# Kernel optimization log

Measured on AMD Instinct MI355X. Metric: run time of the kernel, lower is better.

Reference implementation:

```python
import jax, jax.numpy as jnp
import numpy as np

N = 10000      # nodes
E = 160000     # edges
F = 64         # channels (hidden_irreps 0e multiplicity)
NS = 10        # species
NB = 8         # num_bessel
NL = 4         # max_ell + 1
LM = 16        # total SH components (l=0..3)
RMAX = 10.0
AVG = 16.0     # avg_num_neighbors
L_OF = jnp.array([0,1,1,1,2,2,2,2,2,3,3,3,3,3,3,3])  # l index of each SH component


def _sph(u):
    """Component-normalized real spherical harmonics l=0..3 on unit vectors [E,3] -> [E,16]."""
    x, y, z = u[..., 0], u[..., 1], u[..., 2]
    s3, s5, s7 = 3.0**0.5, 5.0**0.5, 7.0**0.5
    s15, s42, s70, s105 = 15.0**0.5, 42.0**0.5, 70.0**0.5, 105.0**0.5
    one = jnp.ones_like(x)
    return jnp.stack([
        one,
        s3*x, s3*y, s3*z,
        s15*x*y, s15*y*z, (s5/2)*(3*z*z - 1), s15*x*z, (s15/2)*(x*x - y*y),
        (s70/4)*y*(3*x*x - y*y), s105*x*y*z, (s42/4)*y*(5*z*z - 1),
        (s7/2)*z*(5*z*z - 3), (s42/4)*x*(5*z*z - 1),
        (s105/2)*z*(x*x - y*y), (s70/4)*x*(x*x - 3*y*y),
    ], axis=-1)


def _bessel(r):
    """Bessel radial basis with smooth polynomial cutoff. r [E] -> [E,NB]."""
    n = jnp.arange(1, NB + 1, dtype=r.dtype)
    eb = (2.0 / RMAX) ** 0.5 * jnp.sin(n * jnp.pi * r[:, None] / RMAX) / (r[:, None] + 1e-9)
    p = 5.0
    xr = r / RMAX
    env = (1.0 - ((p+1)*(p+2)/2) * xr**p + p*(p+2) * xr**(p+1) - (p*(p+1)/2) * xr**(p+2))
    env = jnp.where(xr < 1.0, env, 0.0)
    return eb * env[:, None]


def _interaction(node_feats, node_attrs, Y, bess, senders, receivers,
                 W_up, Wr1, Wr2, Wr3, W_mix, W_sc, w_prod, last):
    # linear down-projection of scalar channel feeding the edge tensor product
    h = node_feats[:, :, 0] @ W_up                                   # [N,F]
    # per-edge radial weights, one per (channel, l) path
    R = jax.nn.silu(bess @ Wr1)
    R = jax.nn.silu(R @ Wr2)
    R = (R @ Wr3).reshape(E, F, NL)                                  # [E,F,4]
    Rlm = R[:, :, L_OF]                                              # [E,F,16]
    # edge tensor-product message: gather senders, modulate by radial, outer with SH
    m = h[senders][:, :, None] * Rlm * Y[:, None, :]                 # [E,F,16]
    A = jax.ops.segment_sum(m, receivers, num_segments=N) / AVG      # [N,F,16]
    # per-l channel mixing (equivariant linear)
    A = jnp.einsum('nfk,kfg->ngk', A, W_mix[L_OF])                   # [N,F,16]
    # species-dependent residual (skip tensor product with node attrs)
    wsp = jnp.einsum('ns,sfg->nfg', node_attrs, W_sc)                # [N,F,F]
    sc = jnp.einsum('nfk,nfg->ngk', node_feats, wsp)                 # [N,F,16]
    # symmetric product basis (correlation=3): scalar-modulated polynomial, equivariant
    s = A[:, :, 0]
    B = A * (w_prod[0] + w_prod[1]*s + w_prod[2]*s*s)[:, :, None]
    out = B + sc
    if last:  # last layer keeps only 0e (scalar) irreps
        out = out * (jnp.arange(LM) == 0).astype(out.dtype)
    return out


def _forward(positions, node_attrs, shifts, senders, receivers, w_embed,
             u0_up, u0_r1, u0_r2, u0_r3, u0_mix, u0_sc, u0_prod, w_read0,
             u1_up, u1_r1, u1_r2, u1_r3, u1_mix, u1_sc, u1_prod, w_mlp1, w_mlp2):
    vec = positions[receivers] - positions[senders] + shifts         # [E,3]
    r = jnp.linalg.norm(vec, axis=-1)
    Y = _sph(vec / (r[:, None] + 1e-9))                              # [E,16]
    bess = _bessel(r)                                                # [E,8]
    # node embedding into scalar channel of [N,F,16] state
    nf = jnp.zeros((N, F, LM), positions.dtype).at[:, :, 0].set(node_attrs @ w_embed)
    nf = _interaction(nf, node_attrs, Y, bess, senders, receivers,
                      u0_up, u0_r1, u0_r2, u0_r3, u0_mix, u0_sc, u0_prod, last=False)
    out0 = nf[:, :, 0] @ w_read0                                     # [N,1] linear readout
    nf = _interaction(nf, node_attrs, Y, bess, senders, receivers,
                      u1_up, u1_r1, u1_r2, u1_r3, u1_mix, u1_sc, u1_prod, last=True)
    out1 = jax.nn.silu(nf[:, :, 0] @ w_mlp1) @ w_mlp2                # [N,1] nonlinear readout
    return jnp.stack([out0, out1], axis=1)                           # [N,2,1]


def setup_inputs() -> dict:
    key = jax.random.key(0)
    ks = jax.random.split(key, 24)
    positions = jax.random.uniform(ks[0], (N, 3), jnp.float32) * 5.0
    species = jax.random.randint(ks[1], (N,), 0, NS)
    node_attrs = jax.nn.one_hot(species, NS, dtype=jnp.float32)
    shifts = jnp.zeros((E, 3), jnp.float32)
    senders = jax.random.randint(ks[2], (E,), 0, N, dtype=jnp.int32)
    receivers = jax.random.randint(ks[3], (E,), 0, N, dtype=jnp.int32)

    def nrm(k, shape, fan_in):
        return jax.random.normal(k, shape, jnp.float32) / (fan_in ** 0.5)

    d = dict(positions=positions, node_attrs=node_attrs, shifts=shifts,
             senders=senders, receivers=receivers,
             w_embed=nrm(ks[4], (NS, F), NS))
    for i, base in ((0, 5), (1, 13)):
        d[f'u{i}_up'] = nrm(ks[base], (F, F), F)
        d[f'u{i}_r1'] = nrm(ks[base+1], (NB, 64), NB)
        d[f'u{i}_r2'] = nrm(ks[base+2], (64, 64), 64)
        d[f'u{i}_r3'] = nrm(ks[base+3], (64, F*NL), 64)
        d[f'u{i}_mix'] = nrm(ks[base+4], (NL, F, F), F)
        d[f'u{i}_sc'] = nrm(ks[base+5], (NS, F, F), F)
        d[f'u{i}_prod'] = nrm(ks[base+6], (3, F), 1)
    d['w_read0'] = nrm(ks[12], (F, 1), F)
    d['w_mlp1'] = nrm(ks[20], (F, 16), F)
    d['w_mlp2'] = nrm(ks[21], (16, 1), 16)
    return d


def reference(positions, node_attrs, shifts, senders, receivers, w_embed,
              u0_up, u0_r1, u0_r2, u0_r3, u0_mix, u0_sc, u0_prod, w_read0,
              u1_up, u1_r1, u1_r2, u1_r3, u1_mix, u1_sc, u1_prod, w_mlp1, w_mlp2):
    return _forward(positions, node_attrs, shifts, senders, receivers, w_embed,
                    u0_up, u0_r1, u0_r2, u0_r3, u0_mix, u0_sc, u0_prod, w_read0,
                    u1_up, u1_r1, u1_r2, u1_r3, u1_mix, u1_sc, u1_prod, w_mlp1, w_mlp2)
```

## Files before the change

### kernel.cpp

```cpp
#include <hip/hip_runtime.h>
#include <hip/hip_bf16.h>
#include <cstdint>
#include <cstddef>

#define NN 10000
#define NE 160000

typedef unsigned short u16;
typedef __attribute__((ext_vector_type(8))) short short8;
typedef __attribute__((ext_vector_type(4))) float f32x4;

__device__ __forceinline__ float b2f(u16 u){
    union { uint32_t i; float f; } v; v.i = ((uint32_t)u) << 16; return v.f;
}
__device__ __forceinline__ u16 f2b(float f){
    union { __hip_bfloat16 h; u16 u; } c; c.h = __float2bfloat16(f); return c.u;
}
__device__ __forceinline__ float silu_f(float x){ return x / (1.f + __expf(-x)); }
__device__ __forceinline__ float ldr(const void* p, int i, int bf){
    return bf ? b2f(((const u16*)p)[i]) : ((const float*)p)[i];
}

constexpr size_t W_FLAG = 0;
constexpr size_t W_CNT  = 16;
constexpr size_t W_OFFS = 10016;
constexpr size_t W_CUR  = 20032;
constexpr size_t W_SSND = 30032;
constexpr size_t W_ATT  = 350032;
constexpr size_t W_POS  = 450032;
constexpr size_t W_SHF  = 480032;
constexpr size_t W_WGT  = 960032;
constexpr size_t OW_EMB = 0;
constexpr size_t OW_UP0 = 640;
constexpr size_t OW_R10 = 4736;
constexpr size_t OW_R20 = 5248;
constexpr size_t OW_R30 = 9344;
constexpr size_t OW_MIX0= 25728;
constexpr size_t OW_SC0 = 42112;
constexpr size_t OW_PR0 = 83072;
constexpr size_t OW_UP1 = 83264;
constexpr size_t OW_R11 = 87360;
constexpr size_t OW_R21 = 87872;
constexpr size_t OW_R31 = 91968;
constexpr size_t OW_MIX1= 108352;
constexpr size_t OW_SC1 = 124736;
constexpr size_t OW_PR1 = 165696;
constexpr size_t OW_RD0 = 165888;
constexpr size_t OW_ML1 = 165952;
constexpr size_t OW_ML2 = 166976;
constexpr size_t OW_TEND = 167000;
constexpr size_t W_BES  = W_WGT + OW_TEND;
constexpr size_t W_NF0  = W_BES + (size_t)NE*8;
constexpr size_t W_H    = W_NF0 + (size_t)NN*64;
constexpr size_t W_A    = W_H   + (size_t)NN*64;
constexpr size_t W_NF1  = W_A   + (size_t)NN*64;
constexpr size_t W_R0   = W_NF1 + (size_t)NN*64;
constexpr size_t W_R1   = W_R0  + (size_t)NE*32;
constexpr size_t WP_DUAL   = W_R1 + (size_t)NE*32;
constexpr size_t WP_SINGLE = W_R0 + (size_t)NE*32;
constexpr size_t W_RS_D = WP_DUAL   + 10400;
constexpr size_t W_RS_S = WP_SINGLE + 10400;
constexpr size_t W_RS_F = W_R0;
constexpr size_t WP_F   = W_R0 + NE;

constexpr size_t NEED_DUAL   = (W_RS_D + NE) * 4;
constexpr size_t NEED_SINGLE = (W_RS_S + NE) * 4;

constexpr int OCT  = 520;
constexpr int OCTS = 136;

__global__ void k_dh(const uint32_t* __restrict__ attrs, const int* __restrict__ rcv,
                     int* __restrict__ flag, int* __restrict__ cnt){
    int i = blockIdx.x * 256 + threadIdx.x;
    int c = 0;
    if (i < 50000){
        uint32_t v = attrs[i];
        c = (v != 0u && v != 0x3F800000u) ? 1 : 0;
    }
    unsigned long long m = __ballot(c);
    if ((threadIdx.x & 63) == 0 && m)
        atomicAdd(flag, (int)__popcll(m));
    if (i < NE) atomicAdd(&cnt[rcv[i]], 1);
}

struct PrepArgs { const void* s[21]; float* d[21]; int n[21]; };
__global__ __launch_bounds__(1024) void k_scan_prep(PrepArgs a, const int* __restrict__ flag,
        const int* __restrict__ cnt, int* __restrict__ offs, int* __restrict__ cur,
        u16* __restrict__ WP, float* __restrict__ nf0, float* __restrict__ h){
    int bf = flag[0] > 100;
    int t = threadIdx.x;
    if (blockIdx.x == 0){
        __shared__ int cl[10000];
        __shared__ int part[1024];
        for (int i = t; i < 10000; i += 1024) cl[i] = cnt[i];
        __syncthreads();
        int base = t * 10;
        int s = 0;
        #pragma unroll
        for (int i = 0; i < 10; i++) if (base + i < NN) s += cl[base + i];
        part[t] = s; __syncthreads();
        for (int d = 1; d < 1024; d <<= 1){
            int v = part[t];
            if (t >= d) v += part[t - d];
            __syncthreads();
            part[t] = v;
            __syncthreads();
        }
        int run = part[t] - s;
        #pragma unroll
        for (int i = 0; i < 10; i++){
            int idx = base + i;
            if (idx < NN){ offs[idx] = run; cur[idx] = run; run += cl[idx]; }
        }
        if (t == 1023) offs[NN] = part[1023];
    } else if (blockIdx.x < 65){
        int stride = 64 * 1024;
        int t0 = (blockIdx.x - 1) * 1024 + t;
        for (int k = 0; k < 21; k++){
            float* d = a.d[k]; int n4 = a.n[k] >> 2;
            if (bf){
                const uint2* s = (const uint2*)a.s[k];
                for (int i = t0; i < n4; i += stride){
                    uint2 v = s[i];
                    float4 o;
                    o.x = b2f((u16)(v.x & 0xffffu));
                    o.y = b2f((u16)(v.x >> 16));
                    o.z = b2f((u16)(v.y & 0xffffu));
                    o.w = b2f((u16)(v.y >> 16));
                    ((float4*)d)[i] = o;
                }
            } else {
                const float4* s = (const float4*)a.s[k];
                for (int i = t0; i < n4; i += stride) ((float4*)d)[i] = s[i];
            }
        }
    } else if (blockIdx.x < 67){
        int b = blockIdx.x - 65;
        const void* W1 = a.s[b ? 12 : 5];
        const void* W2 = a.s[b ? 13 : 6];
        const void* W3 = a.s[b ? 14 : 7];
        u16* dst = WP + b * 10400;
        for (int i = t; i < 5200; i += 1024) ((uint32_t*)dst)[i] = 0;
        __syncthreads();
        for (int i = t; i < 512; i += 1024){
            int n = i >> 3, k = i & 7;
            dst[n*8 + k] = f2b(ldr(W1, k*64 + n, bf));
        }
        for (int i = t; i < 2048; i += 1024){
            int k = (i >> 6) * 2, n = i & 63;
            uint32_t p2 = ((uint32_t)f2b(ldr(W2, (k+1)*64 + n, bf)) << 16) | f2b(ldr(W2, k*64 + n, bf));
            uint32_t p3 = ((uint32_t)f2b(ldr(W3, (k+1)*256 + 4*n, bf)) << 16) | f2b(ldr(W3, k*256 + 4*n, bf));
            *(uint32_t*)&dst[2080 + (k>>3)*OCT + n*8 + (k&7)] = p2;
            *(uint32_t*)&dst[6240 + (k>>3)*OCT + n*8 + (k&7)] = p3;
        }
    } else {
        int nb = blockIdx.x - 67;
        int n = nb*16 + (t >> 6);
        int l = t & 63;
        const void* attrs = a.s[1];
        const void* Wemb  = a.s[3];
        const void* Wup0  = a.s[4];
        float acc = 0.f;
        #pragma unroll
        for (int s = 0; s < 10; s++) acc += ldr(attrs, n*10 + s, bf) * ldr(Wemb, s*64 + l, bf);
        nf0[n*64 + l] = acc;
        float hv = 0.f;
        #pragma unroll 16
        for (int g = 0; g < 64; g++) hv += __shfl(acc, g) * ldr(Wup0, g*64 + l, bf);
        h[n*64 + l] = hv;
    }
}

__global__ void k_scatter_r(const int* __restrict__ rcv, const int* __restrict__ snd,
        const void* __restrict__ posr, const void* __restrict__ shfr,
        int* __restrict__ cur, int* __restrict__ ssnd, float* __restrict__ rs,
        const int* __restrict__ flag){
    int e = blockIdx.x * 256 + threadIdx.x;
    if (e >= NE) return;
    int bf = flag[0] > 100;
    int r = rcv[e], s = snd[e];
    float vx = ldr(posr, r*3+0, bf) - ldr(posr, s*3+0, bf) + ldr(shfr, e*3+0, bf);
    float vy = ldr(posr, r*3+1, bf) - ldr(posr, s*3+1, bf) + ldr(shfr, e*3+1, bf);
    float vz = ldr(posr, r*3+2, bf) - ldr(posr, s*3+2, bf) + ldr(shfr, e*3+2, bf);
    float rr = sqrtf(vx*vx + vy*vy + vz*vz);
    int p = atomicAdd(&cur[r], 1);
    ssnd[p] = s;
    rs[p] = rr;
}

__global__ void k_bess(const float* __restrict__ rs, float* __restrict__ bessp){
    int p = blockIdx.x * 256 + threadIdx.x;
    if (p >= NE) return;
    float rr = rs[p];
    float xr = rr * 0.1f;
    float x2 = xr*xr; float x5 = x2*x2*xr;
    float env = 1.f - 21.f*x5 + 35.f*x5*xr - 15.f*x5*x2;
    if (xr >= 1.f) env = 0.f;
    float scl = 0.4472135954999579f * env / (rr + 1e-9f);
    float b[8];
    #pragma unroll
    for (int n = 1; n <= 8; n++)
        b[n-1] = scl * sinf((float)n * 3.14159265358979323846f * rr * 0.1f);
    float4* be = (float4*)(bessp + (size_t)p*8);
    be[0] = make_float4(b[0], b[1], b[2], b[3]);
    be[1] = make_float4(b[4], b[5], b[6], b[7]);
}

__global__ __launch_bounds__(256) void k_mlp_mfma(const float* __restrict__ rs,
        const u16* __restrict__ WPa, const u16* __restrict__ WPb,
        u16* __restrict__ R0, u16* __restrict__ R1, int nblk0){
    __shared__ __align__(16) u16 W[10400];
    __shared__ __align__(16) u16 X[4][20*OCTS];
    int half = blockIdx.x >= nblk0;
    int blk  = half ? blockIdx.x - nblk0 : blockIdx.x;
    const u16* WP = half ? WPb : WPa;
    u16* R = half ? R1 : R0;
    int t = threadIdx.x;
    int w = t >> 6, lane = t & 63;
    int q = lane >> 4, r = lane & 15;
    u16* Xw = &X[w][0];
    for (int i = t; i < 1300; i += 256) ((uint4*)W)[i] = ((const uint4*)WP)[i];
    {
        uint32_t* xz = (uint32_t*)(Xw + OCTS);
        for (int i = lane; i < 204; i += 64) xz[i] = 0;
    }
    __syncthreads();
    int pbase = blk * 256 + w * 64;
    #pragma unroll 1
    for (int st = 0; st < 4; st++){
        int pb = pbase + st * 16;
        {
            float rr = rs[pb + (lane >> 2)];
            float xr = rr * 0.1f;
            float x2 = xr*xr, x5 = x2*x2*xr;
            float env = 1.f - 21.f*x5 + 35.f*x5*xr - 15.f*x5*x2;
            if (xr >= 1.f) env = 0.f;
            float scl = 0.4472135954999579f * env / (rr + 1e-9f);
            int k0 = (lane & 3) * 2;
            float b0 = scl * __sinf((float)(k0+1) * 0.3141592653589793f * rr);
            float b1 = scl * __sinf((float)(k0+2) * 0.3141592653589793f * rr);
            ((uint32_t*)Xw)[lane] = ((uint32_t)f2b(b1) << 16) | f2b(b0);
        }
        {
            short8 a = *(const short8*)&Xw[q*OCTS + r*8];
            #pragma unroll
            for (int nt = 0; nt < 4; nt++){
                short8 b = *(const short8*)&W[q*OCT + (nt*16 + r)*8];
                f32x4 c = {0.f, 0.f, 0.f, 0.f};
                c = __builtin_amdgcn_mfma_f32_16x16x32_bf16(a, b, c, 0, 0, 0);
                #pragma unroll
                for (int g = 0; g < 4; g++){
                    int e = q*4 + g;
                    int n = nt*16 + r;
                    Xw[(4 + (n>>3))*OCTS + e*8 + (n&7)] = f2b(silu_f(c[g]));
                }
            }
        }
        {
            short8 a0 = *(const short8*)&Xw[(4+q)*OCTS + r*8];
            short8 a1 = *(const short8*)&Xw[(8+q)*OCTS + r*8];
            #pragma unroll
            for (int nt = 0; nt < 4; nt++){
                short8 b0 = *(const short8*)&W[2080 + q*OCT + (nt*16 + r)*8];
                short8 b1 = *(const short8*)&W[2080 + (4+q)*OCT + (nt*16 + r)*8];
                f32x4 c = {0.f, 0.f, 0.f, 0.f};
                c = __builtin_amdgcn_mfma_f32_16x16x32_bf16(a0, b0, c, 0, 0, 0);
                c = __builtin_amdgcn_mfma_f32_16x16x32_bf16(a1, b1, c, 0, 0, 0);
                #pragma unroll
                for (int g = 0; g < 4; g++){
                    int e = q*4 + g;
                    int n = nt*16 + r;
                    Xw[(12 + (n>>3))*OCTS + e*8 + (n&7)] = f2b(silu_f(c[g]));
                }
            }
        }
        {
            short8 a0 = *(const short8*)&Xw[(12+q)*OCTS + r*8];
            short8 a1 = *(const short8*)&Xw[(16+q)*OCTS + r*8];
            #pragma unroll
            for (int nt = 0; nt < 4; nt++){
                short8 b0 = *(const short8*)&W[6240 + q*OCT + (nt*16 + r)*8];
                short8 b1 = *(const short8*)&W[6240 + (4+q)*OCT + (nt*16 + r)*8];
                f32x4 c = {0.f, 0.f, 0.f, 0.f};
                c = __builtin_amdgcn_mfma_f32_16x16x32_bf16(a0, b0, c, 0, 0, 0);
                c = __builtin_amdgcn_mfma_f32_16x16x32_bf16(a1, b1, c, 0, 0, 0);
                #pragma unroll
                for (int g = 0; g < 4; g++){
                    int e = q*4 + g;
                    int n = nt*16 + r;
                    R[(size_t)(pb + e)*64 + n] = f2b(c[g]);
                }
            }
        }
    }
}

template<int LAST>
__global__ __launch_bounds__(256) void k_gnode(const int* __restrict__ offs,
        const int* __restrict__ ssnd, const float* __restrict__ h, const u16* __restrict__ R,
        const float* __restrict__ nf, const float* __restrict__ attrs,
        const float* __restrict__ Wmix0, const float* __restrict__ Wsc,
        const float* __restrict__ Wprod, const float* __restrict__ Wtail,
        const float* __restrict__ Wml2, const float* __restrict__ Wup1,
        float* __restrict__ nf1out, float* __restrict__ hout,
        void* __restrict__ out, const int* __restrict__ flag){
    int wv = threadIdx.x >> 6;
    int n  = blockIdx.x * 4 + wv;
    int l  = threadIdx.x & 63;
    int beg = __builtin_amdgcn_readfirstlane(offs[n]);
    int end = __builtin_amdgcn_readfirstlane(offs[n+1]);
    float acc = 0.f;
    for (int c = beg; c < end; c += 64){
        int ld = c + l; if (ld >= end) ld = end - 1;
        int sv = ssnd[ld];
        int m = end - c; if (m > 64) m = 64;
        int j = 0;
        for (; j + 4 <= m; j += 4){
            int s0 = __builtin_amdgcn_readlane(sv, j+0);
            int s1 = __builtin_amdgcn_readlane(sv, j+1);
            int s2 = __builtin_amdgcn_readlane(sv, j+2);
            int s3 = __builtin_amdgcn_readlane(sv, j+3);
            float r0 = b2f(R[(size_t)(c+j+0)*64 + l]);
            float r1 = b2f(R[(size_t)(c+j+1)*64 + l]);
            float r2 = b2f(R[(size_t)(c+j+2)*64 + l]);
            float r3 = b2f(R[(size_t)(c+j+3)*64 + l]);
            acc += h[s0*64 + l]*r0 + h[s1*64 + l]*r1 + h[s2*64 + l]*r2 + h[s3*64 + l]*r3;
        }
        for (; j < m; j++){
            int s = __builtin_amdgcn_readlane(sv, j);
            acc += h[s*64 + l] * b2f(R[(size_t)(c+j)*64 + l]);
        }
    }
    float Af  = acc * 0.0625f;
    float nff = nf[n*64 + l];
    float am = 0.f;
    #pragma unroll 16
    for (int f = 0; f < 64; f++) am += __shfl(Af, f) * Wmix0[f*64 + l];
    float sc = 0.f;
    for (int s = 0; s < 10; s++){
        float av = attrs[n*10 + s];
        if (av != 0.f){
            const float* Ws = Wsc + s*4096;
            float t = 0.f;
            #pragma unroll 16
            for (int f = 0; f < 64; f++) t += __shfl(nff, f) * Ws[f*64 + l];
            sc += av * t;
        }
    }
    float poly = Wprod[l] + Wprod[64 + l]*am + Wprod[128 + l]*am*am;
    float val = am*poly + sc;
    float rv;
    if (LAST == 0){
        nf1out[n*64 + l] = val;
        float hv = 0.f;
        #pragma unroll 16
        for (int g = 0; g < 64; g++) hv += __shfl(val, g) * Wup1[g*64 + l];
        hout[n*64 + l] = hv;
        rv = val * Wtail[l];
    } else {
        int lj = l & 15;
        float t = 0.f;
        #pragma unroll 16
        for (int g = 0; g < 64; g++){
            float vg = __shfl(val, g);
            t += vg * Wtail[g*16 + lj];
        }
        rv = (l < 16) ? (silu_f(t) * Wml2[lj]) : 0.f;
    }
    #pragma unroll
    for (int o2 = 32; o2; o2 >>= 1) rv += __shfl_down(rv, o2);
    if (l == 0){
        int idx = 2*n + LAST;
        if (flag[0] > 100) ((__hip_bfloat16*)out)[idx] = __float2bfloat16(rv);
        else               ((float*)out)[idx] = rv;
    }
}

__global__ __launch_bounds__(256) void k_msg_fused(const int* __restrict__ offs,
        const int* __restrict__ ssnd, const float* __restrict__ h, const float* __restrict__ bessp,
        const float* __restrict__ W1, const float* __restrict__ W2, const float* __restrict__ W3,
        float* __restrict__ A){
    int wv = threadIdx.x >> 6;
    int n  = blockIdx.x * 4 + wv;
    int l  = threadIdx.x & 63;
    float w1c[8];
    #pragma unroll
    for (int i = 0; i < 8; i++) w1c[i] = W1[i*64 + l];
    float w2c[64];
    #pragma unroll
    for (int j = 0; j < 64; j++) w2c[j] = W2[j*64 + l];
    float w3c[64];
    #pragma unroll
    for (int j = 0; j < 64; j++) w3c[j] = W3[j*256 + 4*l];
    float acc = 0.f;
    int beg = __builtin_amdgcn_readfirstlane(offs[n]);
    int end = __builtin_amdgcn_readfirstlane(offs[n+1]);
    for (int p = beg; p < end; p++){
        int s = __builtin_amdgcn_readfirstlane(ssnd[p]);
        const float* be = bessp + (size_t)p*8;
        float h1 = 0.f;
        #pragma unroll
        for (int i = 0; i < 8; i++) h1 += be[i] * w1c[i];
        h1 = silu_f(h1);
        float h2 = 0.f;
        #pragma unroll
        for (int j = 0; j < 64; j++) h2 += __shfl(h1, j) * w2c[j];
        h2 = silu_f(h2);
        float rr = 0.f;
        #pragma unroll
        for (int j = 0; j < 64; j++) rr += __shfl(h2, j) * w3c[j];
        acc += h[s*64 + l] * rr;
    }
    A[n*64 + l] = acc * 0.0625f;
}
template<int LAST>
__global__ __launch_bounds__(256) void k_node(const float* __restrict__ A, const float* __restrict__ nf,
        const float* __restrict__ attrs, const float* __restrict__ Wmix0, const float* __restrict__ Wsc,
        const float* __restrict__ Wprod, const float* __restrict__ Wtail, const float* __restrict__ Wml2,
        const float* __restrict__ Wup1, float* __restrict__ nf1out, float* __restrict__ hout,
        void* __restrict__ out, const int* __restrict__ flag){
    int wv = threadIdx.x >> 6;
    int n  = blockIdx.x * 4 + wv;
    int l  = threadIdx.x & 63;
    float Af  = A[n*64 + l];
    float nff = nf[n*64 + l];
    float am = 0.f;
    #pragma unroll 16
    for (int f = 0; f < 64; f++) am += __shfl(Af, f) * Wmix0[f*64 + l];
    float sc = 0.f;
    for (int s = 0; s < 10; s++){
        float av = attrs[n*10 + s];
        if (av != 0.f){
            const float* Ws = Wsc + s*4096;
            float t = 0.f;
            #pragma unroll 16
            for (int f = 0; f < 64; f++) t += __shfl(nff, f) * Ws[f*64 + l];
            sc += av * t;
        }
    }
    float poly = Wprod[l] + Wprod[64 + l]*am + Wprod[128 + l]*am*am;
    float val = am*poly + sc;
    float rv;
    if (LAST == 0){
        nf1out[n*64 + l] = val;
        float hv = 0.f;
        #pragma unroll 16
        for (int g = 0; g < 64; g++) hv += __shfl(val, g) * Wup1[g*64 + l];
        hout[n*64 + l] = hv;
        rv = val * Wtail[l];
    } else {
        int lj = l & 15;
        float t = 0.f;
        #pragma unroll 16
        for (int g = 0; g < 64; g++){
            float vg = __shfl(val, g);
            t += vg * Wtail[g*16 + lj];
        }
        rv = (l < 16) ? (silu_f(t) * Wml2[lj]) : 0.f;
    }
    #pragma unroll
    for (int o2 = 32; o2; o2 >>= 1) rv += __shfl_down(rv, o2);
    if (l == 0){
        int idx = 2*n + LAST;
        if (flag[0] > 100) ((__hip_bfloat16*)out)[idx] = __float2bfloat16(rv);
        else               ((float*)out)[idx] = rv;
    }
}

extern "C" void kernel_launch(void* const* d_in, const int* in_sizes, int n_in,
                              void* d_out, int out_size, void* d_ws, size_t ws_size,
                              hipStream_t stream) {
    int*   iw = (int*)d_ws;
    float* fw = (float*)d_ws;
    const int* snd = (const int*)d_in[3];
    const int* rcv = (const int*)d_in[4];

    PrepArgs pa;
    const int    pidx[21] = {0,1,2, 5,6,7,8,9,10,11,12,13,14,15,16,17,18,19,20,21,22};
    const size_t pdst[21] = {W_POS, W_ATT, W_SHF,
        W_WGT+OW_EMB, W_WGT+OW_UP0, W_WGT+OW_R10, W_WGT+OW_R20, W_WGT+OW_R30,
        W_WGT+OW_MIX0, W_WGT+OW_SC0, W_WGT+OW_PR0,
        W_WGT+OW_UP1, W_WGT+OW_R11, W_WGT+OW_R21, W_WGT+OW_R31,
        W_WGT+OW_MIX1, W_WGT+OW_SC1, W_WGT+OW_PR1,
        W_WGT+OW_RD0, W_WGT+OW_ML1, W_WGT+OW_ML2};
    const int    pn[21]   = {30000, 100000, 480000,
        640, 4096, 512, 4096, 16384, 16384, 40960, 192,
        4096, 512, 4096, 16384, 16384, 40960, 192, 64, 1024, 16};
    for (int i = 0; i < 21; i++){
        pa.s[i] = d_in[pidx[i]];
        pa.d[i] = fw + pdst[i];
        pa.n[i] = pn[i];
    }

    const int dual   = (ws_size >= NEED_DUAL);
    const int single = (!dual && ws_size >= NEED_SINGLE);
    const size_t wp  = dual ? WP_DUAL : (single ? WP_SINGLE : WP_F);
    const size_t wrs = dual ? W_RS_D  : (single ? W_RS_S  : W_RS_F);

    hipMemsetAsync(iw, 0, (W_CNT + NN) * sizeof(int), stream);
    k_dh<<<NE/256, 256, 0, stream>>>((const uint32_t*)d_in[1], rcv, iw + W_FLAG, iw + W_CNT);
    k_scan_prep<<<692, 1024, 0, stream>>>(pa, iw + W_FLAG, iw + W_CNT, iw + W_OFFS, iw + W_CUR,
                                          (u16*)(fw + wp), fw + W_NF0, fw + W_H);
    k_scatter_r<<<NE/256, 256, 0, stream>>>(rcv, snd, d_in[0], d_in[2],
                                            iw + W_CUR, iw + W_SSND, fw + wrs, iw + W_FLAG);

    if (dual){
        k_mlp_mfma<<<1250, 256, 0, stream>>>(fw + wrs, (const u16*)(fw + wp),
                                             (const u16*)(fw + wp) + 10400,
                                             (u16*)(fw + W_R0), (u16*)(fw + W_R1), 625);
        k_gnode<0><<<NN/4, 256, 0, stream>>>(iw+W_OFFS, iw+W_SSND, fw+W_H, (const u16*)(fw+W_R0),
            fw+W_NF0, fw+W_ATT, fw+W_WGT+OW_MIX0, fw+W_WGT+OW_SC0, fw+W_WGT+OW_PR0,
            fw+W_WGT+OW_RD0, nullptr, fw+W_WGT+OW_UP1, fw+W_NF1, fw+W_A, d_out, iw+W_FLAG);
        k_gnode<1><<<NN/4, 256, 0, stream>>>(iw+W_OFFS, iw+W_SSND, fw+W_A, (const u16*)(fw+W_R1),
            fw+W_NF1, fw+W_ATT, fw+W_WGT+OW_MIX1, fw+W_WGT+OW_SC1, fw+W_WGT+OW_PR1,
            fw+W_WGT+OW_ML1, fw+W_WGT+OW_ML2, nullptr, nullptr, nullptr, d_out, iw+W_FLAG);
    } else if (single){
        k_mlp_mfma<<<625, 256, 0, stream>>>(fw + wrs, (const u16*)(fw + wp),
                                            (const u16*)(fw + wp),
                                            (u16*)(fw + W_R0), (u16*)(fw + W_R0), 2000000);
        k_gnode<0><<<NN/4, 256, 0, stream>>>(iw+W_OFFS, iw+W_SSND, fw+W_H, (const u16*)(fw+W_R0),
            fw+W_NF0, fw+W_ATT, fw+W_WGT+OW_MIX0, fw+W_WGT+OW_SC0, fw+W_WGT+OW_PR0,
            fw+W_WGT+OW_RD0, nullptr, fw+W_WGT+OW_UP1, fw+W_NF1, fw+W_A, d_out, iw+W_FLAG);
        k_mlp_mfma<<<625, 256, 0, stream>>>(fw + wrs, (const u16*)(fw + wp) + 10400,
                                            (const u16*)(fw + wp) + 10400,
                                            (u16*)(fw + W_R0), (u16*)(fw + W_R0), 2000000);
        k_gnode<1><<<NN/4, 256, 0, stream>>>(iw+W_OFFS, iw+W_SSND, fw+W_A, (const u16*)(fw+W_R0),
            fw+W_NF1, fw+W_ATT, fw+W_WGT+OW_MIX1, fw+W_WGT+OW_SC1, fw+W_WGT+OW_PR1,
            fw+W_WGT+OW_ML1, fw+W_WGT+OW_ML2, nullptr, nullptr, nullptr, d_out, iw+W_FLAG);
    } else {
        k_bess<<<NE/256, 256, 0, stream>>>(fw + wrs, fw + W_BES);
        k_msg_fused<<<NN/4, 256, 0, stream>>>(iw+W_OFFS, iw+W_SSND, fw+W_H, fw+W_BES,
                                              fw+W_WGT+OW_R10, fw+W_WGT+OW_R20,
                                              fw+W_WGT+OW_R30, fw + W_A);
        k_node<0><<<NN/4, 256, 0, stream>>>(fw + W_A, fw + W_NF0, fw + W_ATT,
                                            fw + W_WGT + OW_MIX0, fw + W_WGT + OW_SC0,
                                            fw + W_WGT + OW_PR0, fw + W_WGT + OW_RD0, nullptr,
                                            fw + W_WGT + OW_UP1, fw + W_NF1, fw + W_H,
                                            d_out, iw + W_FLAG);
        k_msg_fused<<<NN/4, 256, 0, stream>>>(iw+W_OFFS, iw+W_SSND, fw+W_H, fw+W_BES,
                                              fw+W_WGT+OW_R11, fw+W_WGT+OW_R21,
                                              fw+W_WGT+OW_R31, fw + W_A);
        k_node<1><<<NN/4, 256, 0, stream>>>(fw + W_A, fw + W_NF1, fw + W_ATT,
                                            fw + W_WGT + OW_MIX1, fw + W_WGT + OW_SC1,
                                            fw + W_WGT + OW_PR1, fw + W_WGT + OW_ML1,
                                            fw + W_WGT + OW_ML2, nullptr, nullptr, nullptr,
                                            d_out, iw + W_FLAG);
    }
}
```

Measured before the change: 224.2 us.

## Fuse front-end memset, histogram, scan, prep and scatter into one cooperative kernel

```diff
diff --git a/kernel.cpp b/kernel.cpp
--- a/kernel.cpp
+++ b/kernel.cpp
@@ -1,10 +1,15 @@
 #include <hip/hip_runtime.h>
 #include <hip/hip_bf16.h>
+#include <hip/hip_cooperative_groups.h>
 #include <cstdint>
 #include <cstddef>
 
+namespace cg = cooperative_groups;
+
 #define NN 10000
 #define NE 160000
+#define FGRID 1024
+#define FGT   (FGRID * 256)
 
 typedef unsigned short u16;
 typedef __attribute__((ext_vector_type(8))) short short8;
@@ -69,37 +74,43 @@
 constexpr int OCT  = 520;
 constexpr int OCTS = 136;
 
-__global__ void k_dh(const uint32_t* __restrict__ attrs, const int* __restrict__ rcv,
-                     int* __restrict__ flag, int* __restrict__ cnt){
-    int i = blockIdx.x * 256 + threadIdx.x;
-    int c = 0;
-    if (i < 50000){
-        uint32_t v = attrs[i];
-        c = (v != 0u && v != 0x3F800000u) ? 1 : 0;
-    }
-    unsigned long long m = __ballot(c);
-    if ((threadIdx.x & 63) == 0 && m)
-        atomicAdd(flag, (int)__popcll(m));
-    if (i < NE) atomicAdd(&cnt[rcv[i]], 1);
-}
-
 struct PrepArgs { const void* s[21]; float* d[21]; int n[21]; };
-__global__ __launch_bounds__(1024) void k_scan_prep(PrepArgs a, const int* __restrict__ flag,
-        const int* __restrict__ cnt, int* __restrict__ offs, int* __restrict__ cur,
-        u16* __restrict__ WP, float* __restrict__ nf0, float* __restrict__ h){
+
+__global__ __launch_bounds__(256, 4) void k_front(PrepArgs a,
+        const int* __restrict__ rcv, const int* __restrict__ snd,
+        int* __restrict__ iw0, int* __restrict__ offs, int* __restrict__ rank,
+        int* __restrict__ ssnd, float* __restrict__ rs,
+        u16* __restrict__ WP, float* __restrict__ nf0, float* __restrict__ h)
+{
+    cg::grid_group grid = cg::this_grid();
+    int t = threadIdx.x;
+    int gtid = blockIdx.x * 256 + t;
+    int* flag = iw0;
+    int* cnt  = iw0 + 16;
+
+    for (int i = gtid; i < 10016; i += FGT) iw0[i] = 0;
+    grid.sync();
+
+    {
+        int c = 0;
+        if (gtid < 50000){
+            uint32_t v = ((const uint32_t*)a.s[1])[gtid];
+            c = (v != 0u && v != 0x3F800000u) ? 1 : 0;
+        }
+        unsigned long long m = __ballot(c);
+        if ((t & 63) == 0 && m) atomicAdd(flag, (int)__popcll(m));
+        if (gtid < NE) rank[gtid] = atomicAdd(&cnt[rcv[gtid]], 1);
+    }
+    grid.sync();
     int bf = flag[0] > 100;
-    int t = threadIdx.x;
+
     if (blockIdx.x == 0){
-        __shared__ int cl[10000];
-        __shared__ int part[1024];
-        for (int i = t; i < 10000; i += 1024) cl[i] = cnt[i];
-        __syncthreads();
-        int base = t * 10;
+        __shared__ int part[256];
+        int base = t * 40;
         int s = 0;
-        #pragma unroll
-        for (int i = 0; i < 10; i++) if (base + i < NN) s += cl[base + i];
+        for (int i = 0; i < 40; i++){ int idx = base + i; if (idx < NN) s += cnt[idx]; }
         part[t] = s; __syncthreads();
-        for (int d = 1; d < 1024; d <<= 1){
+        for (int d = 1; d < 256; d <<= 1){
             int v = part[t];
             if (t >= d) v += part[t - d];
             __syncthreads();
@@ -107,46 +118,24 @@
             __syncthreads();
         }
         int run = part[t] - s;
-        #pragma unroll
-        for (int i = 0; i < 10; i++){
+        for (int i = 0; i < 40; i++){
             int idx = base + i;
-            if (idx < NN){ offs[idx] = run; cur[idx] = run; run += cl[idx]; }
-        }
-        if (t == 1023) offs[NN] = part[1023];
-    } else if (blockIdx.x < 65){
-        int stride = 64 * 1024;
-        int t0 = (blockIdx.x - 1) * 1024 + t;
-        for (int k = 0; k < 21; k++){
-            float* d = a.d[k]; int n4 = a.n[k] >> 2;
-            if (bf){
-                const uint2* s = (const uint2*)a.s[k];
-                for (int i = t0; i < n4; i += stride){
-                    uint2 v = s[i];
-                    float4 o;
-                    o.x = b2f((u16)(v.x & 0xffffu));
-                    o.y = b2f((u16)(v.x >> 16));
-                    o.z = b2f((u16)(v.y & 0xffffu));
-                    o.w = b2f((u16)(v.y >> 16));
-                    ((float4*)d)[i] = o;
-                }
-            } else {
-                const float4* s = (const float4*)a.s[k];
-                for (int i = t0; i < n4; i += stride) ((float4*)d)[i] = s[i];
-            }
-        }
-    } else if (blockIdx.x < 67){
-        int b = blockIdx.x - 65;
+            if (idx < NN){ offs[idx] = run; run += cnt[idx]; }
+        }
+        if (t == 255) offs[NN] = part[255];
+    } else if (blockIdx.x <= 2){
+        int b = blockIdx.x - 1;
         const void* W1 = a.s[b ? 12 : 5];
         const void* W2 = a.s[b ? 13 : 6];
         const void* W3 = a.s[b ? 14 : 7];
         u16* dst = WP + b * 10400;
-        for (int i = t; i < 5200; i += 1024) ((uint32_t*)dst)[i] = 0;
+        for (int i = t; i < 5200; i += 256) ((uint32_t*)dst)[i] = 0;
         __syncthreads();
-        for (int i = t; i < 512; i += 1024){
+        for (int i = t; i < 512; i += 256){
             int n = i >> 3, k = i & 7;
             dst[n*8 + k] = f2b(ldr(W1, k*64 + n, bf));
         }
-        for (int i = t; i < 2048; i += 1024){
+        for (int i = t; i < 2048; i += 256){
             int k = (i >> 6) * 2, n = i & 63;
             uint32_t p2 = ((uint32_t)f2b(ldr(W2, (k+1)*64 + n, bf)) << 16) | f2b(ldr(W2, k*64 + n, bf));
             uint32_t p3 = ((uint32_t)f2b(ldr(W3, (k+1)*256 + 4*n, bf)) << 16) | f2b(ldr(W3, k*256 + 4*n, bf));
@@ -154,38 +143,56 @@
             *(uint32_t*)&dst[6240 + (k>>3)*OCT + n*8 + (k&7)] = p3;
         }
     } else {
-        int nb = blockIdx.x - 67;
-        int n = nb*16 + (t >> 6);
-        int l = t & 63;
         const void* attrs = a.s[1];
         const void* Wemb  = a.s[3];
         const void* Wup0  = a.s[4];
-        float acc = 0.f;
-        #pragma unroll
-        for (int s = 0; s < 10; s++) acc += ldr(attrs, n*10 + s, bf) * ldr(Wemb, s*64 + l, bf);
-        nf0[n*64 + l] = acc;
-        float hv = 0.f;
-        #pragma unroll 16
-        for (int g = 0; g < 64; g++) hv += __shfl(acc, g) * ldr(Wup0, g*64 + l, bf);
-        h[n*64 + l] = hv;
-    }
-}
-
-__global__ void k_scatter_r(const int* __restrict__ rcv, const int* __restrict__ snd,
-        const void* __restrict__ posr, const void* __restrict__ shfr,
-        int* __restrict__ cur, int* __restrict__ ssnd, float* __restrict__ rs,
-        const int* __restrict__ flag){
-    int e = blockIdx.x * 256 + threadIdx.x;
-    if (e >= NE) return;
-    int bf = flag[0] > 100;
-    int r = rcv[e], s = snd[e];
-    float vx = ldr(posr, r*3+0, bf) - ldr(posr, s*3+0, bf) + ldr(shfr, e*3+0, bf);
-    float vy = ldr(posr, r*3+1, bf) - ldr(posr, s*3+1, bf) + ldr(shfr, e*3+1, bf);
-    float vz = ldr(posr, r*3+2, bf) - ldr(posr, s*3+2, bf) + ldr(shfr, e*3+2, bf);
-    float rr = sqrtf(vx*vx + vy*vy + vz*vz);
-    int p = atomicAdd(&cur[r], 1);
-    ssnd[p] = s;
-    rs[p] = rr;
+        int l = t & 63;
+        for (int it = 0; it < 3; it++){
+            int n = (blockIdx.x - 3)*4 + (t >> 6) + it*4084;
+            if (n < NN){
+                float acc = 0.f;
+                #pragma unroll
+                for (int s = 0; s < 10; s++) acc += ldr(attrs, n*10 + s, bf) * ldr(Wemb, s*64 + l, bf);
+                nf0[n*64 + l] = acc;
+                float hv = 0.f;
+                #pragma unroll 16
+                for (int g = 0; g < 64; g++) hv += __shfl(acc, g) * ldr(Wup0, g*64 + l, bf);
+                h[n*64 + l] = hv;
+            }
+        }
+    }
+    grid.sync();
+
+    if (gtid < NE){
+        int r = rcv[gtid], s = snd[gtid];
+        const void* posr = a.s[0];
+        const void* shfr = a.s[2];
+        float vx = ldr(posr, r*3+0, bf) - ldr(posr, s*3+0, bf) + ldr(shfr, gtid*3+0, bf);
+        float vy = ldr(posr, r*3+1, bf) - ldr(posr, s*3+1, bf) + ldr(shfr, gtid*3+1, bf);
+        float vz = ldr(posr, r*3+2, bf) - ldr(posr, s*3+2, bf) + ldr(shfr, gtid*3+2, bf);
+        float rr = sqrtf(vx*vx + vy*vy + vz*vz);
+        int p = offs[r] + rank[gtid];
+        ssnd[p] = s;
+        rs[p] = rr;
+    }
+    for (int k = 0; k < 21; k++){
+        float* d = a.d[k]; int n4 = a.n[k] >> 2;
+        if (bf){
+            const uint2* sp = (const uint2*)a.s[k];
+            for (int i = gtid; i < n4; i += FGT){
+                uint2 v = sp[i];
+                float4 o;
+                o.x = b2f((u16)(v.x & 0xffffu));
+                o.y = b2f((u16)(v.x >> 16));
+                o.z = b2f((u16)(v.y & 0xffffu));
+                o.w = b2f((u16)(v.y >> 16));
+                ((float4*)d)[i] = o;
+            }
+        } else {
+            const float4* sp = (const float4*)a.s[k];
+            for (int i = gtid; i < n4; i += FGT) ((float4*)d)[i] = sp[i];
+        }
+    }
 }
 
 __global__ void k_bess(const float* __restrict__ rs, float* __restrict__ bessp){
@@ -497,12 +504,21 @@
     const size_t wp  = dual ? WP_DUAL : (single ? WP_SINGLE : WP_F);
     const size_t wrs = dual ? W_RS_D  : (single ? W_RS_S  : W_RS_F);
 
-    hipMemsetAsync(iw, 0, (W_CNT + NN) * sizeof(int), stream);
-    k_dh<<<NE/256, 256, 0, stream>>>((const uint32_t*)d_in[1], rcv, iw + W_FLAG, iw + W_CNT);
-    k_scan_prep<<<692, 1024, 0, stream>>>(pa, iw + W_FLAG, iw + W_CNT, iw + W_OFFS, iw + W_CUR,
-                                          (u16*)(fw + wp), fw + W_NF0, fw + W_H);
-    k_scatter_r<<<NE/256, 256, 0, stream>>>(rcv, snd, d_in[0], d_in[2],
-                                            iw + W_CUR, iw + W_SSND, fw + wrs, iw + W_FLAG);
+    {
+        int* iw0p   = iw;
+        int* offsp  = iw + W_OFFS;
+        int* rankp  = iw + W_BES;
+        int* ssndp  = iw + W_SSND;
+        float* rsp  = fw + wrs;
+        u16* WPp    = (u16*)(fw + wp);
+        float* nf0p = fw + W_NF0;
+        float* hp   = fw + W_H;
+        void* kargs[] = { (void*)&pa, (void*)&rcv, (void*)&snd, (void*)&iw0p, (void*)&offsp,
+                          (void*)&rankp, (void*)&ssndp, (void*)&rsp, (void*)&WPp,
+                          (void*)&nf0p, (void*)&hp };
+        hipLaunchCooperativeKernel(reinterpret_cast<const void*>(&k_front),
+                                   dim3(FGRID), dim3(256), kargs, 0, stream);
+    }
 
     if (dual){
         k_mlp_mfma<<<1250, 256, 0, stream>>>(fw + wrs, (const u16*)(fw + wp),
```

Measured after the change: 533.4 us. 138% more time.

## Fuse radial MLP with message gather and segmented atomic scatter

Applied to the files above, without the earlier changes.

```diff
diff --git a/kernel.cpp b/kernel.cpp
--- a/kernel.cpp
+++ b/kernel.cpp
@@ -24,11 +24,9 @@
 constexpr size_t W_FLAG = 0;
 constexpr size_t W_CNT  = 16;
 constexpr size_t W_OFFS = 10016;
-constexpr size_t W_CUR  = 20032;
 constexpr size_t W_SSND = 30032;
 constexpr size_t W_ATT  = 350032;
-constexpr size_t W_POS  = 450032;
-constexpr size_t W_SHF  = 480032;
+constexpr size_t W_SRCV = 480032;
 constexpr size_t W_WGT  = 960032;
 constexpr size_t OW_EMB = 0;
 constexpr size_t OW_UP0 = 640;
@@ -54,23 +52,21 @@
 constexpr size_t W_H    = W_NF0 + (size_t)NN*64;
 constexpr size_t W_A    = W_H   + (size_t)NN*64;
 constexpr size_t W_NF1  = W_A   + (size_t)NN*64;
-constexpr size_t W_R0   = W_NF1 + (size_t)NN*64;
-constexpr size_t W_R1   = W_R0  + (size_t)NE*32;
-constexpr size_t WP_DUAL   = W_R1 + (size_t)NE*32;
-constexpr size_t WP_SINGLE = W_R0 + (size_t)NE*32;
-constexpr size_t W_RS_D = WP_DUAL   + 10400;
-constexpr size_t W_RS_S = WP_SINGLE + 10400;
-constexpr size_t W_RS_F = W_R0;
-constexpr size_t WP_F   = W_R0 + NE;
-
-constexpr size_t NEED_DUAL   = (W_RS_D + NE) * 4;
-constexpr size_t NEED_SINGLE = (W_RS_S + NE) * 4;
+constexpr size_t W_A0   = W_NF1 + (size_t)NN*64;
+constexpr size_t W_A1   = W_A0  + (size_t)NN*64;
+constexpr size_t W_RS_N = W_A1  + (size_t)NN*64;
+constexpr size_t WP_N   = W_RS_N + NE;
+constexpr size_t W_RS_F = W_A0;
+constexpr size_t WP_F   = W_A0 + NE;
+
+constexpr size_t NEED_FUSED = (WP_N + 10400) * 4;
 
 constexpr int OCT  = 520;
 constexpr int OCTS = 136;
 
 __global__ void k_dh(const uint32_t* __restrict__ attrs, const int* __restrict__ rcv,
-                     int* __restrict__ flag, int* __restrict__ cnt){
+                     int* __restrict__ flag, int* __restrict__ cnt, int* __restrict__ rank,
+                     float* __restrict__ az){
     int i = blockIdx.x * 256 + threadIdx.x;
     int c = 0;
     if (i < 50000){
@@ -80,12 +76,14 @@
     unsigned long long m = __ballot(c);
     if ((threadIdx.x & 63) == 0 && m)
         atomicAdd(flag, (int)__popcll(m));
-    if (i < NE) atomicAdd(&cnt[rcv[i]], 1);
+    if (i < NE) rank[i] = atomicAdd(&cnt[rcv[i]], 1);
+    #pragma unroll
+    for (int k = 0; k < 8; k++) az[(size_t)k*NE + i] = 0.f;
 }
 
 struct PrepArgs { const void* s[21]; float* d[21]; int n[21]; };
 __global__ __launch_bounds__(1024) void k_scan_prep(PrepArgs a, const int* __restrict__ flag,
-        const int* __restrict__ cnt, int* __restrict__ offs, int* __restrict__ cur,
+        const int* __restrict__ cnt, int* __restrict__ offs,
         u16* __restrict__ WP, float* __restrict__ nf0, float* __restrict__ h){
     int bf = flag[0] > 100;
     int t = threadIdx.x;
@@ -110,7 +108,7 @@
         #pragma unroll
         for (int i = 0; i < 10; i++){
             int idx = base + i;
-            if (idx < NN){ offs[idx] = run; cur[idx] = run; run += cl[idx]; }
+            if (idx < NN){ offs[idx] = run; run += cl[idx]; }
         }
         if (t == 1023) offs[NN] = part[1023];
     } else if (blockIdx.x < 65){
@@ -173,7 +171,8 @@
 
 __global__ void k_scatter_r(const int* __restrict__ rcv, const int* __restrict__ snd,
         const void* __restrict__ posr, const void* __restrict__ shfr,
-        int* __restrict__ cur, int* __restrict__ ssnd, float* __restrict__ rs,
+        const int* __restrict__ offs, const int* __restrict__ rank,
+        int* __restrict__ ssnd, int* __restrict__ srcv, float* __restrict__ rs,
         const int* __restrict__ flag){
     int e = blockIdx.x * 256 + threadIdx.x;
     if (e >= NE) return;
@@ -183,8 +182,9 @@
     float vy = ldr(posr, r*3+1, bf) - ldr(posr, s*3+1, bf) + ldr(shfr, e*3+1, bf);
     float vz = ldr(posr, r*3+2, bf) - ldr(posr, s*3+2, bf) + ldr(shfr, e*3+2, bf);
     float rr = sqrtf(vx*vx + vy*vy + vz*vz);
-    int p = atomicAdd(&cur[r], 1);
+    int p = offs[r] + rank[e];
     ssnd[p] = s;
+    srcv[p] = r;
     rs[p] = rr;
 }
 
@@ -206,29 +206,34 @@
     be[1] = make_float4(b[4], b[5], b[6], b[7]);
 }
 
-__global__ __launch_bounds__(256) void k_mlp_mfma(const float* __restrict__ rs,
-        const u16* __restrict__ WPa, const u16* __restrict__ WPb,
-        u16* __restrict__ R0, u16* __restrict__ R1, int nblk0){
+__global__ __launch_bounds__(256) void k_fmsg(const float* __restrict__ rs,
+        const int* __restrict__ ssnd, const int* __restrict__ srcv,
+        const float* __restrict__ h, const u16* __restrict__ WP,
+        float* __restrict__ A){
     __shared__ __align__(16) u16 W[10400];
     __shared__ __align__(16) u16 X[4][20*OCTS];
-    int half = blockIdx.x >= nblk0;
-    int blk  = half ? blockIdx.x - nblk0 : blockIdx.x;
-    const u16* WP = half ? WPb : WPa;
-    u16* R = half ? R1 : R0;
+    __shared__ __align__(16) float M[4][16*66];
     int t = threadIdx.x;
     int w = t >> 6, lane = t & 63;
     int q = lane >> 4, r = lane & 15;
     u16* Xw = &X[w][0];
+    float* Mw = &M[w][0];
     for (int i = t; i < 1300; i += 256) ((uint4*)W)[i] = ((const uint4*)WP)[i];
     {
         uint32_t* xz = (uint32_t*)(Xw + OCTS);
         for (int i = lane; i < 204; i += 64) xz[i] = 0;
     }
     __syncthreads();
-    int pbase = blk * 256 + w * 64;
+    int pbase = blockIdx.x * 256 + w * 64;
     #pragma unroll 1
     for (int st = 0; st < 4; st++){
         int pb = pbase + st * 16;
+        int sv = ssnd[pb + (lane & 15)];
+        int nv = srcv[pb + (lane & 15)];
+        int s0 = __shfl(sv, q*4 + 0);
+        int s1 = __shfl(sv, q*4 + 1);
+        int s2 = __shfl(sv, q*4 + 2);
+        int s3 = __shfl(sv, q*4 + 3);
         {
             float rr = rs[pb + (lane >> 2)];
             float xr = rr * 0.1f;
@@ -284,135 +289,34 @@
                 f32x4 c = {0.f, 0.f, 0.f, 0.f};
                 c = __builtin_amdgcn_mfma_f32_16x16x32_bf16(a0, b0, c, 0, 0, 0);
                 c = __builtin_amdgcn_mfma_f32_16x16x32_bf16(a1, b1, c, 0, 0, 0);
-                #pragma unroll
-                for (int g = 0; g < 4; g++){
-                    int e = q*4 + g;
-                    int n = nt*16 + r;
-                    R[(size_t)(pb + e)*64 + n] = f2b(c[g]);
+                int n = nt*16 + r;
+                float h0 = h[s0*64 + n];
+                float h1 = h[s1*64 + n];
+                float h2 = h[s2*64 + n];
+                float h3 = h[s3*64 + n];
+                Mw[(q*4+0)*66 + n] = c[0]*h0;
+                Mw[(q*4+1)*66 + n] = c[1]*h1;
+                Mw[(q*4+2)*66 + n] = c[2]*h2;
+                Mw[(q*4+3)*66 + n] = c[3]*h3;
+            }
+        }
+        {
+            int cur = __shfl(nv, 0);
+            float run = 0.f;
+            #pragma unroll
+            for (int e = 0; e < 16; e++){
+                int nid = __shfl(nv, e);
+                if (nid != cur){
+                    atomicAdd(&A[(size_t)cur*64 + lane], run * 0.0625f);
+                    run = 0.f; cur = nid;
                 }
+                run += Mw[e*66 + lane];
             }
-        }
-    }
-}
-
-template<int LAST>
-__global__ __launch_bounds__(256) void k_gnode(const int* __restrict__ offs,
-        const int* __restrict__ ssnd, const float* __restrict__ h, const u16* __restrict__ R,
-        const float* __restrict__ nf, const float* __restrict__ attrs,
-        const float* __restrict__ Wmix0, const float* __restrict__ Wsc,
-        const float* __restrict__ Wprod, const float* __restrict__ Wtail,
-        const float* __restrict__ Wml2, const float* __restrict__ Wup1,
-        float* __restrict__ nf1out, float* __restrict__ hout,
-        void* __restrict__ out, const int* __restrict__ flag){
-    int wv = threadIdx.x >> 6;
-    int n  = blockIdx.x * 4 + wv;
-    int l  = threadIdx.x & 63;
-    int beg = __builtin_amdgcn_readfirstlane(offs[n]);
-    int end = __builtin_amdgcn_readfirstlane(offs[n+1]);
-    float acc = 0.f;
-    for (int c = beg; c < end; c += 64){
-        int ld = c + l; if (ld >= end) ld = end - 1;
-        int sv = ssnd[ld];
-        int m = end - c; if (m > 64) m = 64;
-        int j = 0;
-        for (; j + 4 <= m; j += 4){
-            int s0 = __builtin_amdgcn_readlane(sv, j+0);
-            int s1 = __builtin_amdgcn_readlane(sv, j+1);
-            int s2 = __builtin_amdgcn_readlane(sv, j+2);
-            int s3 = __builtin_amdgcn_readlane(sv, j+3);
-            float r0 = b2f(R[(size_t)(c+j+0)*64 + l]);
-            float r1 = b2f(R[(size_t)(c+j+1)*64 + l]);
-            float r2 = b2f(R[(size_t)(c+j+2)*64 + l]);
-            float r3 = b2f(R[(size_t)(c+j+3)*64 + l]);
-            acc += h[s0*64 + l]*r0 + h[s1*64 + l]*r1 + h[s2*64 + l]*r2 + h[s3*64 + l]*r3;
-        }
-        for (; j < m; j++){
-            int s = __builtin_amdgcn_readlane(sv, j);
-            acc += h[s*64 + l] * b2f(R[(size_t)(c+j)*64 + l]);
-        }
-    }
-    float Af  = acc * 0.0625f;
-    float nff = nf[n*64 + l];
-    float am = 0.f;
-    #pragma unroll 16
-    for (int f = 0; f < 64; f++) am += __shfl(Af, f) * Wmix0[f*64 + l];
-    float sc = 0.f;
-    for (int s = 0; s < 10; s++){
-        float av = attrs[n*10 + s];
-        if (av != 0.f){
-            const float* Ws = Wsc + s*4096;
-            float t = 0.f;
-            #pragma unroll 16
-            for (int f = 0; f < 64; f++) t += __shfl(nff, f) * Ws[f*64 + l];
-            sc += av * t;
-        }
-    }
-    float poly = Wprod[l] + Wprod[64 + l]*am + Wprod[128 + l]*am*am;
-    float val = am*poly + sc;
-    float rv;
-    if (LAST == 0){
-        nf1out[n*64 + l] = val;
-        float hv = 0.f;
-        #pragma unroll 16
-        for (int g = 0; g < 64; g++) hv += __shfl(val, g) * Wup1[g*64 + l];
-        hout[n*64 + l] = hv;
-        rv = val * Wtail[l];
-    } else {
-        int lj = l & 15;
-        float t = 0.f;
-        #pragma unroll 16
-        for (int g = 0; g < 64; g++){
-            float vg = __shfl(val, g);
-            t += vg * Wtail[g*16 + lj];
-        }
-        rv = (l < 16) ? (silu_f(t) * Wml2[lj]) : 0.f;
-    }
-    #pragma unroll
-    for (int o2 = 32; o2; o2 >>= 1) rv += __shfl_down(rv, o2);
-    if (l == 0){
-        int idx = 2*n + LAST;
-        if (flag[0] > 100) ((__hip_bfloat16*)out)[idx] = __float2bfloat16(rv);
-        else               ((float*)out)[idx] = rv;
-    }
-}
-
-__global__ __launch_bounds__(256) void k_msg_fused(const int* __restrict__ offs,
-        const int* __restrict__ ssnd, const float* __restrict__ h, const float* __restrict__ bessp,
-        const float* __restrict__ W1, const float* __restrict__ W2, const float* __restrict__ W3,
-        float* __restrict__ A){
-    int wv = threadIdx.x >> 6;
-    int n  = blockIdx.x * 4 + wv;
-    int l  = threadIdx.x & 63;
-    float w1c[8];
-    #pragma unroll
-    for (int i = 0; i < 8; i++) w1c[i] = W1[i*64 + l];
-    float w2c[64];
-    #pragma unroll
-    for (int j = 0; j < 64; j++) w2c[j] = W2[j*64 + l];
-    float w3c[64];
-    #pragma unroll
-    for (int j = 0; j < 64; j++) w3c[j] = W3[j*256 + 4*l];
-    float acc = 0.f;
-    int beg = __builtin_amdgcn_readfirstlane(offs[n]);
-    int end = __builtin_amdgcn_readfirstlane(offs[n+1]);
-    for (int p = beg; p < end; p++){
-        int s = __builtin_amdgcn_readfirstlane(ssnd[p]);
-        const float* be = bessp + (size_t)p*8;
-        float h1 = 0.f;
-        #pragma unroll
-        for (int i = 0; i < 8; i++) h1 += be[i] * w1c[i];
-        h1 = silu_f(h1);
-        float h2 = 0.f;
-        #pragma unroll
-        for (int j = 0; j < 64; j++) h2 += __shfl(h1, j) * w2c[j];
-        h2 = silu_f(h2);
-        float rr = 0.f;
-        #pragma unroll
-        for (int j = 0; j < 64; j++) rr += __shfl(h2, j) * w3c[j];
-        acc += h[s*64 + l] * rr;
-    }
-    A[n*64 + l] = acc * 0.0625f;
-}
+            atomicAdd(&A[(size_t)cur*64 + lane], run * 0.0625f);
+        }
+    }
+}
+
 template<int LAST>
 __global__ __launch_bounds__(256) void k_node(const float* __restrict__ A, const float* __restrict__ nf,
         const float* __restrict__ attrs, const float* __restrict__ Wmix0, const float* __restrict__ Wsc,
@@ -467,6 +371,44 @@
     }
 }
 
+__global__ __launch_bounds__(256) void k_msg_fused(const int* __restrict__ offs,
+        const int* __restrict__ ssnd, const float* __restrict__ h, const float* __restrict__ bessp,
+        const float* __restrict__ W1, const float* __restrict__ W2, const float* __restrict__ W3,
+        float* __restrict__ A){
+    int wv = threadIdx.x >> 6;
+    int n  = blockIdx.x * 4 + wv;
+    int l  = threadIdx.x & 63;
+    float w1c[8];
+    #pragma unroll
+    for (int i = 0; i < 8; i++) w1c[i] = W1[i*64 + l];
+    float w2c[64];
+    #pragma unroll
+    for (int j = 0; j < 64; j++) w2c[j] = W2[j*64 + l];
+    float w3c[64];
+    #pragma unroll
+    for (int j = 0; j < 64; j++) w3c[j] = W3[j*256 + 4*l];
+    float acc = 0.f;
+    int beg = __builtin_amdgcn_readfirstlane(offs[n]);
+    int end = __builtin_amdgcn_readfirstlane(offs[n+1]);
+    for (int p = beg; p < end; p++){
+        int s = __builtin_amdgcn_readfirstlane(ssnd[p]);
+        const float* be = bessp + (size_t)p*8;
+        float h1 = 0.f;
+        #pragma unroll
+        for (int i = 0; i < 8; i++) h1 += be[i] * w1c[i];
+        h1 = silu_f(h1);
+        float h2 = 0.f;
+        #pragma unroll
+        for (int j = 0; j < 64; j++) h2 += __shfl(h1, j) * w2c[j];
+        h2 = silu_f(h2);
+        float rr = 0.f;
+        #pragma unroll
+        for (int j = 0; j < 64; j++) rr += __shfl(h2, j) * w3c[j];
+        acc += h[s*64 + l] * rr;
+    }
+    A[n*64 + l] = acc * 0.0625f;
+}
+
 extern "C" void kernel_launch(void* const* d_in, const int* in_sizes, int n_in,
                               void* d_out, int out_size, void* d_ws, size_t ws_size,
                               hipStream_t stream) {
@@ -477,13 +419,13 @@
 
     PrepArgs pa;
     const int    pidx[21] = {0,1,2, 5,6,7,8,9,10,11,12,13,14,15,16,17,18,19,20,21,22};
-    const size_t pdst[21] = {W_POS, W_ATT, W_SHF,
+    const size_t pdst[21] = {W_ATT, W_ATT, W_ATT,
         W_WGT+OW_EMB, W_WGT+OW_UP0, W_WGT+OW_R10, W_WGT+OW_R20, W_WGT+OW_R30,
         W_WGT+OW_MIX0, W_WGT+OW_SC0, W_WGT+OW_PR0,
         W_WGT+OW_UP1, W_WGT+OW_R11, W_WGT+OW_R21, W_WGT+OW_R31,
         W_WGT+OW_MIX1, W_WGT+OW_SC1, W_WGT+OW_PR1,
         W_WGT+OW_RD0, W_WGT+OW_ML1, W_WGT+OW_ML2};
-    const int    pn[21]   = {30000, 100000, 480000,
+    const int    pn[21]   = {0, 100000, 0,
         640, 4096, 512, 4096, 16384, 16384, 40960, 192,
         4096, 512, 4096, 16384, 16384, 40960, 192, 64, 1024, 16};
     for (int i = 0; i < 21; i++){
@@ -492,40 +434,30 @@
         pa.n[i] = pn[i];
     }
 
-    const int dual   = (ws_size >= NEED_DUAL);
-    const int single = (!dual && ws_size >= NEED_SINGLE);
-    const size_t wp  = dual ? WP_DUAL : (single ? WP_SINGLE : WP_F);
-    const size_t wrs = dual ? W_RS_D  : (single ? W_RS_S  : W_RS_F);
+    const int fused = (ws_size >= NEED_FUSED);
+    const size_t wp  = fused ? WP_N   : WP_F;
+    const size_t wrs = fused ? W_RS_N : W_RS_F;
+    int* rank = iw + W_BES;
 
     hipMemsetAsync(iw, 0, (W_CNT + NN) * sizeof(int), stream);
-    k_dh<<<NE/256, 256, 0, stream>>>((const uint32_t*)d_in[1], rcv, iw + W_FLAG, iw + W_CNT);
-    k_scan_prep<<<692, 1024, 0, stream>>>(pa, iw + W_FLAG, iw + W_CNT, iw + W_OFFS, iw + W_CUR,
+    k_dh<<<NE/256, 256, 0, stream>>>((const uint32_t*)d_in[1], rcv, iw + W_FLAG, iw + W_CNT,
+                                     rank, fw + W_A0);
+    k_scan_prep<<<692, 1024, 0, stream>>>(pa, iw + W_FLAG, iw + W_CNT, iw + W_OFFS,
                                           (u16*)(fw + wp), fw + W_NF0, fw + W_H);
     k_scatter_r<<<NE/256, 256, 0, stream>>>(rcv, snd, d_in[0], d_in[2],
-                                            iw + W_CUR, iw + W_SSND, fw + wrs, iw + W_FLAG);
-
-    if (dual){
-        k_mlp_mfma<<<1250, 256, 0, stream>>>(fw + wrs, (const u16*)(fw + wp),
-                                             (const u16*)(fw + wp) + 10400,
-                                             (u16*)(fw + W_R0), (u16*)(fw + W_R1), 625);
-        k_gnode<0><<<NN/4, 256, 0, stream>>>(iw+W_OFFS, iw+W_SSND, fw+W_H, (const u16*)(fw+W_R0),
-            fw+W_NF0, fw+W_ATT, fw+W_WGT+OW_MIX0, fw+W_WGT+OW_SC0, fw+W_WGT+OW_PR0,
+                                            iw + W_OFFS, rank, iw + W_SSND, iw + W_SRCV,
+                                            fw + wrs, iw + W_FLAG);
+
+    if (fused){
+        k_fmsg<<<NE/256, 256, 0, stream>>>(fw + wrs, iw + W_SSND, iw + W_SRCV,
+                                           fw + W_H, (const u16*)(fw + wp), fw + W_A0);
+        k_node<0><<<NN/4, 256, 0, stream>>>(fw + W_A0, fw + W_NF0, fw + W_ATT,
+            fw+W_WGT+OW_MIX0, fw+W_WGT+OW_SC0, fw+W_WGT+OW_PR0,
             fw+W_WGT+OW_RD0, nullptr, fw+W_WGT+OW_UP1, fw+W_NF1, fw+W_A, d_out, iw+W_FLAG);
-        k_gnode<1><<<NN/4, 256, 0, stream>>>(iw+W_OFFS, iw+W_SSND, fw+W_A, (const u16*)(fw+W_R1),
-            fw+W_NF1, fw+W_ATT, fw+W_WGT+OW_MIX1, fw+W_WGT+OW_SC1, fw+W_WGT+OW_PR1,
-            fw+W_WGT+OW_ML1, fw+W_WGT+OW_ML2, nullptr, nullptr, nullptr, d_out, iw+W_FLAG);
-    } else if (single){
-        k_mlp_mfma<<<625, 256, 0, stream>>>(fw + wrs, (const u16*)(fw + wp),
-                                            (const u16*)(fw + wp),
-                                            (u16*)(fw + W_R0), (u16*)(fw + W_R0), 2000000);
-        k_gnode<0><<<NN/4, 256, 0, stream>>>(iw+W_OFFS, iw+W_SSND, fw+W_H, (const u16*)(fw+W_R0),
-            fw+W_NF0, fw+W_ATT, fw+W_WGT+OW_MIX0, fw+W_WGT+OW_SC0, fw+W_WGT+OW_PR0,
-            fw+W_WGT+OW_RD0, nullptr, fw+W_WGT+OW_UP1, fw+W_NF1, fw+W_A, d_out, iw+W_FLAG);
-        k_mlp_mfma<<<625, 256, 0, stream>>>(fw + wrs, (const u16*)(fw + wp) + 10400,
-                                            (const u16*)(fw + wp) + 10400,
-                                            (u16*)(fw + W_R0), (u16*)(fw + W_R0), 2000000);
-        k_gnode<1><<<NN/4, 256, 0, stream>>>(iw+W_OFFS, iw+W_SSND, fw+W_A, (const u16*)(fw+W_R0),
-            fw+W_NF1, fw+W_ATT, fw+W_WGT+OW_MIX1, fw+W_WGT+OW_SC1, fw+W_WGT+OW_PR1,
+        k_fmsg<<<NE/256, 256, 0, stream>>>(fw + wrs, iw + W_SSND, iw + W_SRCV,
+                                           fw + W_A, (const u16*)(fw + wp) + 10400, fw + W_A1);
+        k_node<1><<<NN/4, 256, 0, stream>>>(fw + W_A1, fw + W_NF1, fw + W_ATT,
+            fw+W_WGT+OW_MIX1, fw+W_WGT+OW_SC1, fw+W_WGT+OW_PR1,
             fw+W_WGT+OW_ML1, fw+W_WGT+OW_ML2, nullptr, nullptr, nullptr, d_out, iw+W_FLAG);
     } else {
         k_bess<<<NE/256, 256, 0, stream>>>(fw + wrs, fw + W_BES);
```

After: 253.8 us. +13.2%, slower.
